# Kernel optimization log

Measured on AMD Instinct MI355X. Metric: run time of the kernel, lower is better.

Reference implementation:

```python
import jax, jax.numpy as jnp
import numpy as np

B, KLEN, QLEN = 16, 4096, 1
D_MODEL, HEADS, KERNELS = 1024, 8, 10
DIM = D_MODEL // HEADS  # 128
SCALE = 0.02


def setup_inputs() -> dict:
    key = jax.random.key(0)
    ks = jax.random.split(key, 12)
    return {
        "query": jax.random.normal(ks[0], (B, QLEN, D_MODEL), jnp.float32),
        "key_in": jax.random.normal(ks[1], (B, KLEN, D_MODEL), jnp.float32),
        "value": jax.random.normal(ks[2], (B, KLEN, D_MODEL), jnp.float32),
        "prev_align": jax.random.uniform(ks[3], (B, HEADS, KLEN), jnp.float32),
        # learned params
        "conv_w": jax.random.normal(ks[4], (KERNELS, HEADS, 3), jnp.float32) * SCALE,   # OIH, k=3
        "conv_b": jnp.zeros((KERNELS,), jnp.float32),
        "w_u": jax.random.normal(ks[5], (KERNELS, DIM), jnp.float32) * SCALE,
        "w_q": jax.random.normal(ks[6], (D_MODEL, HEADS * DIM), jnp.float32) * SCALE,
        "w_v": jax.random.normal(ks[7], (D_MODEL, HEADS * DIM), jnp.float32) * SCALE,
        "bias": jax.random.uniform(ks[8], (DIM,), jnp.float32, minval=-0.1, maxval=0.1),
        "score_w": jax.random.normal(ks[9], (DIM,), jnp.float32) * SCALE,
        "score_b": jnp.zeros((), jnp.float32),
    }


def reference(query, key_in, value, prev_align, conv_w, conv_b, w_u, w_q, w_v, bias, score_w, score_b):
    b, k_len = key_in.shape[0], key_in.shape[1]
    # location features: conv1d over k_len with heads as channels -> [B, KERNELS, k_len]
    loc = jax.lax.conv_general_dilated(
        prev_align, conv_w, window_strides=(1,), padding=[(1, 1)],
        dimension_numbers=("NCH", "OIH", "NCH")) + conv_b[None, :, None]
    loc_energy = jnp.tanh(jnp.einsum("bck,cd->bkd", loc, w_u))  # [B, k_len, DIM]
    # projections split into heads
    q = jnp.einsum("bqf,fe->bqe", query, w_q).reshape(b, QLEN, HEADS, DIM).transpose(0, 2, 1, 3)   # [B,H,1,DIM]
    k = jnp.einsum("bkf,fe->bke", key_in, w_v).reshape(b, k_len, HEADS, DIM).transpose(0, 2, 1, 3)  # [B,H,K,DIM]
    v = value.reshape(b, k_len, HEADS, DIM).transpose(0, 2, 1, 3)                                   # [B,H,K,DIM]
    # additive energy (q_len==1 broadcasts over keys)
    e = jnp.tanh(k + q + loc_energy[:, None] + bias)            # [B,H,K,DIM]
    score = jnp.einsum("bhkd,d->bhk", e, score_w) + score_b    # [B,H,K]
    align = jax.nn.softmax(score, axis=-1)
    context = jnp.einsum("bhk,bhkd->bhd", align, v).reshape(b * HEADS, DIM)
    return context, align
```

## Files before the change

kernel.cpp:

```cpp
#include <hip/hip_runtime.h>
#include <hip/hip_bf16.h>
#include <cstdint>

typedef __attribute__((ext_vector_type(8))) short bf16x8;
typedef __attribute__((ext_vector_type(4))) float f32x4;
typedef __attribute__((ext_vector_type(8))) unsigned short u16x8;
typedef __attribute__((ext_vector_type(4))) unsigned int u32x4;

__device__ __forceinline__ unsigned short f2bf(float f) {
    unsigned int u = __float_as_uint(f);
    unsigned int r = (u + 0x7fffu + ((u >> 16) & 1u)) >> 16;
    return (unsigned short)r;
}

__device__ __forceinline__ float tanh_fast(float x) {
    return 1.0f - 2.0f / (__expf(2.0f * x) + 1.0f);
}

#define GLDS(SRC, DST) __builtin_amdgcn_global_load_lds(                         \
        (const __attribute__((address_space(1))) void*)(SRC),                    \
        (__attribute__((address_space(3))) void*)(DST), 16, 0, 0)

__global__ __launch_bounds__(256) void wv_tile_kernel(
        const float* __restrict__ wv, unsigned short* __restrict__ out) {
    __shared__ float tile[32][129];
    const int h = blockIdx.x;
    const int kt = blockIdx.y;
    const int t = threadIdx.x;
    for (int i = t; i < 1024; i += 256) {
        const int fl = i >> 5;
        const int e4 = (i & 31) * 4;
        const float4 v = *reinterpret_cast<const float4*>(
            wv + (size_t)(kt * 32 + fl) * 1024 + h * 128 + e4);
        tile[fl][e4 + 0] = v.x; tile[fl][e4 + 1] = v.y;
        tile[fl][e4 + 2] = v.z; tile[fl][e4 + 3] = v.w;
    }
    __syncthreads();
#pragma unroll
    for (int cc2 = 0; cc2 < 2; ++cc2) {
        const int c = cc2 * 256 + t;
        const int cb = c >> 6, kg = (c >> 4) & 3, ccl = c & 15;
        const int e_local = cb * 16 + ccl;
        u16x8 u;
#pragma unroll
        for (int jj = 0; jj < 8; ++jj) u[jj] = f2bf(tile[kg * 8 + jj][e_local]);
        *reinterpret_cast<u16x8*>(out + (((size_t)h * 32 + kt) * 512 + c) * 8) = u;
    }
}

__global__ __launch_bounds__(128) void qproj_kernel(
        const float* __restrict__ query, const float* __restrict__ w_q,
        float* __restrict__ ws_q) {
    __shared__ float qs[1024];
    const int bh = blockIdx.x;
    const int b = bh >> 3, h = bh & 7;
    const int t = threadIdx.x;
    for (int i = t; i < 1024; i += 128) qs[i] = query[(size_t)b * 1024 + i];
    __syncthreads();
    float acc = 0.f;
    const float* wcol = w_q + h * 128 + t;
    for (int f = 0; f < 1024; ++f) acc = fmaf(qs[f], wcol[(size_t)f * 1024], acc);
    ws_q[(size_t)bh * 128 + t] = acc;
}

__global__ __launch_bounds__(256) void loc_le_kernel(
        const float* __restrict__ pa, const float* __restrict__ conv_w,
        const float* __restrict__ conv_b, const float* __restrict__ w_u,
        float* __restrict__ le) {
    __shared__ float pas[8][132];
    __shared__ float wu_s[10][128];
    __shared__ float cw[240];
    __shared__ float cb[16];
    const int b = blockIdx.x, k0 = blockIdx.y * 128;
    const int t = threadIdx.x;
    for (int i = t; i < 8 * 130; i += 256) {
        const int hh = i / 130, kk = i % 130;
        const int gk = k0 + kk - 1;
        pas[hh][kk] = (gk >= 0 && gk < 4096) ? pa[((size_t)(b * 8 + hh)) * 4096 + gk] : 0.f;
    }
    for (int i = t; i < 1280; i += 256) wu_s[i >> 7][i & 127] = w_u[i];
    if (t < 240) cw[t] = conv_w[t];
    if (t < 10) cb[t] = conv_b[t];
    __syncthreads();
    const int k = t >> 1;
    const int d0 = (t & 1) * 64;
    float lc[10];
#pragma unroll
    for (int c = 0; c < 10; ++c) {
        float acc = cb[c];
#pragma unroll
        for (int hh = 0; hh < 8; ++hh) {
            acc += pas[hh][k] * cw[(c * 8 + hh) * 3 + 0]
                 + pas[hh][k + 1] * cw[(c * 8 + hh) * 3 + 1]
                 + pas[hh][k + 2] * cw[(c * 8 + hh) * 3 + 2];
        }
        lc[c] = acc;
    }
    float* dst = le + ((size_t)(b * 4096) + k0 + k) * 128 + d0;
#pragma unroll
    for (int dd = 0; dd < 64; dd += 4) {
        float4 o;
#pragma unroll
        for (int jj = 0; jj < 4; ++jj) {
            float s = 0.f;
#pragma unroll
            for (int c = 0; c < 10; ++c) s += lc[c] * wu_s[c][d0 + dd + jj];
            ((float*)&o)[jj] = tanh_fast(s);
        }
        *reinterpret_cast<float4*>(dst + dd) = o;
    }
}

#define NT 32
__global__ __launch_bounds__(512) void gemm_score_kernel(
        const float* __restrict__ key_in, const unsigned short* __restrict__ wvT_tiled,
        const float* __restrict__ le,
        const float* __restrict__ ws_q, const float* __restrict__ bias,
        const float* __restrict__ score_w, const float* __restrict__ score_b,
        float* __restrict__ align_out) {
    __shared__ __align__(16) unsigned short As[3][4096];
    __shared__ __align__(16) unsigned short Bs[3][8192];
    __shared__ float qb_sm[256], sw_sm[128];
    __shared__ float partial[128][4];

    const int t = threadIdx.x;
    const int lane = t & 63, wid = t >> 6;
    const int wm = wid >> 2;
    const int wn = wid & 3;

    const int fid = blockIdx.x;
    const int x = fid & 7, j = fid >> 3;
    const int bm = x * 64 + (j >> 2);
    const int hp = j & 3;
    const int b = bm >> 5;
    const int kk0 = (bm & 31) << 7;

    if (t < 256) {
        const int hh = t >> 7, d = t & 127;
        qb_sm[t] = ws_q[(size_t)(b * 8 + hp * 2 + hh) * 128 + d] + bias[d];
        if (t < 128) sw_sm[t] = score_w[t];
    }

    const int r_ = t >> 2, ks = t & 3;
    const float* aRow = key_in + ((size_t)(b * 4096 + kk0) + r_) * 1024 + ks * 8;
    const int cW = (t >> 6) * 64 + ks * 16 + (r_ & 15);
    const int dst0 = (cW ^ (ks | ((ks & 1) << 2))) * 8;

    const int kgR = lane >> 4;
    const int laneSwz = lane ^ (kgR | ((kgR & 1) << 2));

    const unsigned short* bT = wvT_tiled
        + (size_t)(hp * 2 + (t >> 8)) * 131072 + (t & 255) * 8;
    const int dstB = (t >> 8) * 4096 + (t & 255) * 8;

    float4 st0, st1;

#define LOADA(KT) {                                                               \
        const float* p_ = aRow + (KT) * 32;                                       \
        st0 = *reinterpret_cast<const float4*>(p_);                               \
        st1 = *reinterpret_cast<const float4*>(p_ + 4); }

#define WRITEA(BUF) {                                                             \
        __hip_bfloat162 h0_ = __float22bfloat162_rn({st0.x, st0.y});              \
        __hip_bfloat162 h1_ = __float22bfloat162_rn({st0.z, st0.w});              \
        __hip_bfloat162 h2_ = __float22bfloat162_rn({st1.x, st1.y});              \
        __hip_bfloat162 h3_ = __float22bfloat162_rn({st1.z, st1.w});              \
        u32x4 u_;                                                                 \
        u_[0] = *reinterpret_cast<unsigned int*>(&h0_);                           \
        u_[1] = *reinterpret_cast<unsigned int*>(&h1_);                           \
        u_[2] = *reinterpret_cast<unsigned int*>(&h2_);                           \
        u_[3] = *reinterpret_cast<unsigned int*>(&h3_);                           \
        *reinterpret_cast<u32x4*>(&As[BUF][dst0]) = u_; }

#define STAGE_B(BUF, KT) {                                                        \
        GLDS(bT + (size_t)(KT) * 4096, &Bs[BUF][dstB]);                           \
        GLDS(bT + (size_t)(KT) * 4096 + 2048, &Bs[BUF][dstB + 2048]); }

    f32x4 acc[4][4] = {};

    LOADA(0);
    STAGE_B(0, 0);
    WRITEA(0);
    LOADA(1);

    for (int kt = 0; kt < NT; ++kt) {
        const int cur = kt % 3;
        const int nxt = (kt + 1) % 3;
        STAGE_B(nxt, (kt + 1) & (NT - 1));
        WRITEA(nxt);
        LOADA((kt + 2) & (NT - 1));
        asm volatile("s_waitcnt lgkmcnt(0)\n\t"
                     "s_barrier" ::: "memory");

        bf16x8 af[4], bg[4];
#pragma unroll
        for (int mf = 0; mf < 4; ++mf)
            af[mf] = *reinterpret_cast<const bf16x8*>(
                &As[cur][((wm * 4 + mf) * 64 + laneSwz) * 8]);
#pragma unroll
        for (int nf = 0; nf < 4; ++nf)
            bg[nf] = *reinterpret_cast<const bf16x8*>(
                &Bs[cur][(wn >> 1) * 4096 + ((wn & 1) * 4 + nf) * 512 + lane * 8]);
        __builtin_amdgcn_s_setprio(1);
#pragma unroll
        for (int mf = 0; mf < 4; ++mf)
#pragma unroll
            for (int nf = 0; nf < 4; ++nf)
                acc[mf][nf] = __builtin_amdgcn_mfma_f32_16x16x32_bf16(
                    af[mf], bg[nf], acc[mf][nf], 0, 0, 0);
        __builtin_amdgcn_s_setprio(0);
    }

    const float K2 = 2.8853900817779268f;
    const float sb = score_b[0];
    const int g = lane >> 4;
    const int l15 = lane & 15;
    float kqb[4], swv[4];
#pragma unroll
    for (int nf = 0; nf < 4; ++nf) {
        const int d128 = (wn & 1) * 64 + nf * 16 + l15;
        kqb[nf] = qb_sm[(wn >> 1) * 128 + d128] * K2;
        swv[nf] = sw_sm[d128];
    }
    const float* leB = le + ((size_t)(b * 4096 + kk0) + wm * 64 + g * 4) * 128
                       + (wn & 1) * 64 + l15;

#pragma unroll
    for (int mf = 0; mf < 4; ++mf) {
        float lv[16];
#pragma unroll
        for (int jj = 0; jj < 4; ++jj)
#pragma unroll
            for (int nf = 0; nf < 4; ++nf)
                lv[jj * 4 + nf] = leB[(size_t)(mf * 16 + jj) * 128 + nf * 16];
#pragma unroll
        for (int jj = 0; jj < 4; ++jj) {
            const int row_l = wm * 64 + mf * 16 + g * 4 + jj;
            float sum = 0.f;
#pragma unroll
            for (int nf = 0; nf < 4; ++nf) {
                const float m = fmaf(K2, lv[jj * 4 + nf], kqb[nf]);
                const float tt = fmaf(K2, acc[mf][nf][jj], m);
                const float y = __builtin_amdgcn_exp2f(tt);
                const float r = fmaf(-2.0f, __builtin_amdgcn_rcpf(y + 1.0f), 1.0f);
                sum = fmaf(r, swv[nf], sum);
            }
            sum += __shfl_xor(sum, 1);
            sum += __shfl_xor(sum, 2);
            sum += __shfl_xor(sum, 4);
            sum += __shfl_xor(sum, 8);
            if (l15 == 0) partial[row_l][wn] = sum;
        }
    }
    __syncthreads();
    if (t < 256) {
        const int r = t >> 1, hh = t & 1;
        const float sc = partial[r][hh * 2] + partial[r][hh * 2 + 1] + sb;
        align_out[(size_t)(b * 8 + hp * 2 + hh) * 4096 + kk0 + r] = sc;
    }
}

__global__ __launch_bounds__(256) void softmax_kernel(float* __restrict__ align_o) {
    const int bh = blockIdx.x;
    float* row = align_o + (size_t)bh * 4096;
    const int t = threadIdx.x;
    float v[16];
    float m = -1e30f;
#pragma unroll
    for (int i = 0; i < 16; ++i) {
        v[i] = row[i * 256 + t];
        m = fmaxf(m, v[i]);
    }
#pragma unroll
    for (int off = 32; off; off >>= 1) m = fmaxf(m, __shfl_xor(m, off));
    __shared__ float sm[4], ss[4];
    const int wid = t >> 6;
    if ((t & 63) == 0) sm[wid] = m;
    __syncthreads();
    m = fmaxf(fmaxf(sm[0], sm[1]), fmaxf(sm[2], sm[3]));
    float s = 0.f;
#pragma unroll
    for (int i = 0; i < 16; ++i) {
        v[i] = __expf(v[i] - m);
        s += v[i];
    }
#pragma unroll
    for (int off = 32; off; off >>= 1) s += __shfl_xor(s, off);
    if ((t & 63) == 0) ss[wid] = s;
    __syncthreads();
    s = ss[0] + ss[1] + ss[2] + ss[3];
    const float inv = 1.f / s;
#pragma unroll
    for (int i = 0; i < 16; ++i) row[i * 256 + t] = v[i] * inv;
}

__global__ __launch_bounds__(256) void ctx_partial_kernel(
        const float* __restrict__ value, const float* __restrict__ align_o,
        float* __restrict__ pctx) {
    const int s = blockIdx.x;
    const int bh = blockIdx.y;
    const int b = bh >> 3, h = bh & 7;
    const int t = threadIdx.x;
    const int d4 = (t & 31) * 4;
    const int kg = t >> 5;
    const float* arow = align_o + (size_t)bh * 4096 + s * 128;
    const float* vbase = value + ((size_t)(b * 4096 + s * 128)) * 1024 + h * 128 + d4;
    float4 acc = {0.f, 0.f, 0.f, 0.f};
    for (int i = 0; i < 16; ++i) {
        const int kk = i * 8 + kg;
        const float a = arow[kk];
        const float4 v = *reinterpret_cast<const float4*>(vbase + (size_t)kk * 1024);
        acc.x += a * v.x; acc.y += a * v.y; acc.z += a * v.z; acc.w += a * v.w;
    }
    __shared__ float sm2[8][128];
    *reinterpret_cast<float4*>(&sm2[kg][d4]) = acc;
    __syncthreads();
    if (t < 128) {
        float s0 = 0.f;
#pragma unroll
        for (int gg = 0; gg < 8; ++gg) s0 += sm2[gg][t];
        pctx[((size_t)bh * 32 + s) * 128 + t] = s0;
    }
}

__global__ __launch_bounds__(128) void ctx_reduce_kernel(
        const float* __restrict__ pctx, float* __restrict__ out) {
    const int bh = blockIdx.x;
    const int t = threadIdx.x;
    float acc = 0.f;
    for (int s2 = 0; s2 < 32; ++s2) acc += pctx[((size_t)bh * 32 + s2) * 128 + t];
    out[(size_t)bh * 128 + t] = acc;
}

extern "C" void kernel_launch(void* const* d_in, const int* in_sizes, int n_in,
                              void* d_out, int out_size, void* d_ws, size_t ws_size,
                              hipStream_t stream) {
    const float* query   = (const float*)d_in[0];
    const float* key_in  = (const float*)d_in[1];
    const float* value   = (const float*)d_in[2];
    const float* pa      = (const float*)d_in[3];
    const float* conv_w  = (const float*)d_in[4];
    const float* conv_b  = (const float*)d_in[5];
    const float* w_u     = (const float*)d_in[6];
    const float* w_q     = (const float*)d_in[7];
    const float* w_v     = (const float*)d_in[8];
    const float* bias    = (const float*)d_in[9];
    const float* score_w = (const float*)d_in[10];
    const float* score_b = (const float*)d_in[11];

    float* out = (float*)d_out;
    float* ctx_out = out;
    float* align_out = out + 16384;

    char* ws = (char*)d_ws;
    const size_t OFF_Q    = 0;
    const size_t OFF_WVT  = 65536;
    const size_t OFF_PCTX = OFF_WVT + 2097152;
    const size_t OFF_LE   = OFF_PCTX + 2097152;

    float* ws_q            = (float*)(ws + OFF_Q);
    unsigned short* ws_wvT = (unsigned short*)(ws + OFF_WVT);
    float* ws_pctx         = (float*)(ws + OFF_PCTX);
    float* ws_le           = (float*)(ws + OFF_LE);

    hipLaunchKernelGGL(wv_tile_kernel, dim3(8, 32), dim3(256), 0, stream, w_v, ws_wvT);
    hipLaunchKernelGGL(qproj_kernel, dim3(128), dim3(128), 0, stream, query, w_q, ws_q);
    hipLaunchKernelGGL(loc_le_kernel, dim3(16, 32), dim3(256), 0, stream,
                       pa, conv_w, conv_b, w_u, ws_le);
    hipLaunchKernelGGL(gemm_score_kernel, dim3(2048), dim3(512), 0, stream,
                       key_in, ws_wvT, ws_le, ws_q, bias, score_w, score_b, align_out);
    hipLaunchKernelGGL(softmax_kernel, dim3(128), dim3(256), 0, stream, align_out);
    hipLaunchKernelGGL(ctx_partial_kernel, dim3(32, 128), dim3(256), 0, stream, value, align_out, ws_pctx);
    hipLaunchKernelGGL(ctx_reduce_kernel, dim3(128), dim3(128), 0, stream, ws_pctx, ctx_out);
}
```

Measured before the change: 302.8 us.

## Merge prep kernels into one launch and deepen B-tile prefetch to two stages

Folds the W_v tiling, query projection, and location-energy kernels into one launch that branches on block index, removing two launch gaps and letting the three independent jobs run together. In the GEMM main loop, the B-tile async global-to-LDS copy is now issued two iterations ahead, after the barrier, using the third buffer. This gives the copy more time in flight before it is needed. It depends on the existing lgkmcnt wait and barrier being enough to order the async LDS writes against reads of the buffer being refilled.

```diff
diff --git a/kernel.cpp b/kernel.cpp
--- a/kernel.cpp
+++ b/kernel.cpp
@@ -21,93 +21,95 @@
         (const __attribute__((address_space(1))) void*)(SRC),                    \
         (__attribute__((address_space(3))) void*)(DST), 16, 0, 0)
 
-__global__ __launch_bounds__(256) void wv_tile_kernel(
-        const float* __restrict__ wv, unsigned short* __restrict__ out) {
-    __shared__ float tile[32][129];
-    const int h = blockIdx.x;
-    const int kt = blockIdx.y;
-    const int t = threadIdx.x;
-    for (int i = t; i < 1024; i += 256) {
-        const int fl = i >> 5;
-        const int e4 = (i & 31) * 4;
-        const float4 v = *reinterpret_cast<const float4*>(
-            wv + (size_t)(kt * 32 + fl) * 1024 + h * 128 + e4);
-        tile[fl][e4 + 0] = v.x; tile[fl][e4 + 1] = v.y;
-        tile[fl][e4 + 2] = v.z; tile[fl][e4 + 3] = v.w;
-    }
-    __syncthreads();
-#pragma unroll
-    for (int cc2 = 0; cc2 < 2; ++cc2) {
-        const int c = cc2 * 256 + t;
-        const int cb = c >> 6, kg = (c >> 4) & 3, ccl = c & 15;
-        const int e_local = cb * 16 + ccl;
-        u16x8 u;
-#pragma unroll
-        for (int jj = 0; jj < 8; ++jj) u[jj] = f2bf(tile[kg * 8 + jj][e_local]);
-        *reinterpret_cast<u16x8*>(out + (((size_t)h * 32 + kt) * 512 + c) * 8) = u;
-    }
-}
-
-__global__ __launch_bounds__(128) void qproj_kernel(
+__global__ __launch_bounds__(256) void prep_kernel(
+        const float* __restrict__ wv, unsigned short* __restrict__ wvT,
         const float* __restrict__ query, const float* __restrict__ w_q,
-        float* __restrict__ ws_q) {
-    __shared__ float qs[1024];
-    const int bh = blockIdx.x;
-    const int b = bh >> 3, h = bh & 7;
-    const int t = threadIdx.x;
-    for (int i = t; i < 1024; i += 128) qs[i] = query[(size_t)b * 1024 + i];
-    __syncthreads();
-    float acc = 0.f;
-    const float* wcol = w_q + h * 128 + t;
-    for (int f = 0; f < 1024; ++f) acc = fmaf(qs[f], wcol[(size_t)f * 1024], acc);
-    ws_q[(size_t)bh * 128 + t] = acc;
-}
-
-__global__ __launch_bounds__(256) void loc_le_kernel(
+        float* __restrict__ ws_q,
         const float* __restrict__ pa, const float* __restrict__ conv_w,
         const float* __restrict__ conv_b, const float* __restrict__ w_u,
         float* __restrict__ le) {
-    __shared__ float pas[8][132];
-    __shared__ float wu_s[10][128];
-    __shared__ float cw[240];
-    __shared__ float cb[16];
-    const int b = blockIdx.x, k0 = blockIdx.y * 128;
-    const int t = threadIdx.x;
-    for (int i = t; i < 8 * 130; i += 256) {
-        const int hh = i / 130, kk = i % 130;
-        const int gk = k0 + kk - 1;
-        pas[hh][kk] = (gk >= 0 && gk < 4096) ? pa[((size_t)(b * 8 + hh)) * 4096 + gk] : 0.f;
-    }
-    for (int i = t; i < 1280; i += 256) wu_s[i >> 7][i & 127] = w_u[i];
-    if (t < 240) cw[t] = conv_w[t];
-    if (t < 10) cb[t] = conv_b[t];
-    __syncthreads();
-    const int k = t >> 1;
-    const int d0 = (t & 1) * 64;
-    float lc[10];
-#pragma unroll
-    for (int c = 0; c < 10; ++c) {
-        float acc = cb[c];
-#pragma unroll
-        for (int hh = 0; hh < 8; ++hh) {
-            acc += pas[hh][k] * cw[(c * 8 + hh) * 3 + 0]
-                 + pas[hh][k + 1] * cw[(c * 8 + hh) * 3 + 1]
-                 + pas[hh][k + 2] * cw[(c * 8 + hh) * 3 + 2];
-        }
-        lc[c] = acc;
-    }
-    float* dst = le + ((size_t)(b * 4096) + k0 + k) * 128 + d0;
-#pragma unroll
-    for (int dd = 0; dd < 64; dd += 4) {
-        float4 o;
-#pragma unroll
-        for (int jj = 0; jj < 4; ++jj) {
-            float s = 0.f;
-#pragma unroll
-            for (int c = 0; c < 10; ++c) s += lc[c] * wu_s[c][d0 + dd + jj];
-            ((float*)&o)[jj] = tanh_fast(s);
-        }
-        *reinterpret_cast<float4*>(dst + dd) = o;
+    __shared__ __align__(16) char smem[16640];
+    const int bid = blockIdx.x;
+    const int t = threadIdx.x;
+
+    if (bid < 256) {
+        float (*tile)[129] = reinterpret_cast<float(*)[129]>(smem);
+        const int h = bid >> 5, kt = bid & 31;
+        for (int i = t; i < 1024; i += 256) {
+            const int fl = i >> 5;
+            const int e4 = (i & 31) * 4;
+            const float4 v = *reinterpret_cast<const float4*>(
+                wv + (size_t)(kt * 32 + fl) * 1024 + h * 128 + e4);
+            tile[fl][e4 + 0] = v.x; tile[fl][e4 + 1] = v.y;
+            tile[fl][e4 + 2] = v.z; tile[fl][e4 + 3] = v.w;
+        }
+        __syncthreads();
+#pragma unroll
+        for (int cc2 = 0; cc2 < 2; ++cc2) {
+            const int c = cc2 * 256 + t;
+            const int cb = c >> 6, kg = (c >> 4) & 3, ccl = c & 15;
+            const int e_local = cb * 16 + ccl;
+            u16x8 u;
+#pragma unroll
+            for (int jj = 0; jj < 8; ++jj) u[jj] = f2bf(tile[kg * 8 + jj][e_local]);
+            *reinterpret_cast<u16x8*>(wvT + (((size_t)h * 32 + kt) * 512 + c) * 8) = u;
+        }
+    } else if (bid < 384) {
+        float* qs = reinterpret_cast<float*>(smem);
+        const int bh = bid - 256;
+        const int b = bh >> 3, h = bh & 7;
+        for (int i = t; i < 1024; i += 256) qs[i] = query[(size_t)b * 1024 + i];
+        __syncthreads();
+        if (t < 128) {
+            float acc = 0.f;
+            const float* wcol = w_q + h * 128 + t;
+            for (int f = 0; f < 1024; ++f) acc = fmaf(qs[f], wcol[(size_t)f * 1024], acc);
+            ws_q[(size_t)bh * 128 + t] = acc;
+        }
+    } else {
+        float* pas = reinterpret_cast<float*>(smem);
+        float* wu_s = pas + 1056;
+        float* cw = wu_s + 1280;
+        float* cb = cw + 240;
+        const int idx = bid - 384;
+        const int b = idx >> 5, k0 = (idx & 31) * 128;
+        for (int i = t; i < 8 * 130; i += 256) {
+            const int hh = i / 130, kk = i % 130;
+            const int gk = k0 + kk - 1;
+            pas[hh * 132 + kk] = (gk >= 0 && gk < 4096)
+                ? pa[((size_t)(b * 8 + hh)) * 4096 + gk] : 0.f;
+        }
+        for (int i = t; i < 1280; i += 256) wu_s[i] = w_u[i];
+        if (t < 240) cw[t] = conv_w[t];
+        if (t < 10) cb[t] = conv_b[t];
+        __syncthreads();
+        const int k = t >> 1;
+        const int d0 = (t & 1) * 64;
+        float lc[10];
+#pragma unroll
+        for (int c = 0; c < 10; ++c) {
+            float acc = cb[c];
+#pragma unroll
+            for (int hh = 0; hh < 8; ++hh) {
+                acc += pas[hh * 132 + k] * cw[(c * 8 + hh) * 3 + 0]
+                     + pas[hh * 132 + k + 1] * cw[(c * 8 + hh) * 3 + 1]
+                     + pas[hh * 132 + k + 2] * cw[(c * 8 + hh) * 3 + 2];
+            }
+            lc[c] = acc;
+        }
+        float* dst = le + ((size_t)(b * 4096) + k0 + k) * 128 + d0;
+#pragma unroll
+        for (int dd = 0; dd < 64; dd += 4) {
+            float4 o;
+#pragma unroll
+            for (int jj = 0; jj < 4; ++jj) {
+                float s = 0.f;
+#pragma unroll
+                for (int c = 0; c < 10; ++c) s += lc[c] * wu_s[c * 128 + d0 + dd + jj];
+                ((float*)&o)[jj] = tanh_fast(s);
+            }
+            *reinterpret_cast<float4*>(dst + dd) = o;
+        }
     }
 }
 
@@ -180,17 +182,19 @@
 
     LOADA(0);
     STAGE_B(0, 0);
+    STAGE_B(1, 1);
     WRITEA(0);
     LOADA(1);
 
     for (int kt = 0; kt < NT; ++kt) {
         const int cur = kt % 3;
         const int nxt = (kt + 1) % 3;
-        STAGE_B(nxt, (kt + 1) & (NT - 1));
+        const int pre = (kt + 2) % 3;
         WRITEA(nxt);
         LOADA((kt + 2) & (NT - 1));
         asm volatile("s_waitcnt lgkmcnt(0)\n\t"
                      "s_barrier" ::: "memory");
+        STAGE_B(pre, (kt + 2) & (NT - 1));
 
         bf16x8 af[4], bg[4];
 #pragma unroll
@@ -363,9 +367,8 @@
     float* ws_pctx         = (float*)(ws + OFF_PCTX);
     float* ws_le           = (float*)(ws + OFF_LE);
 
-    hipLaunchKernelGGL(wv_tile_kernel, dim3(8, 32), dim3(256), 0, stream, w_v, ws_wvT);
-    hipLaunchKernelGGL(qproj_kernel, dim3(128), dim3(128), 0, stream, query, w_q, ws_q);
-    hipLaunchKernelGGL(loc_le_kernel, dim3(16, 32), dim3(256), 0, stream,
+    hipLaunchKernelGGL(prep_kernel, dim3(896), dim3(256), 0, stream,
+                       w_v, ws_wvT, query, w_q, ws_q,
                        pa, conv_w, conv_b, w_u, ws_le);
     hipLaunchKernelGGL(gemm_score_kernel, dim3(2048), dim3(512), 0, stream,
                        key_in, ws_wvT, ws_le, ws_q, bias, score_w, score_b, align_out);
```

Result: no change. 297.8 us (-1.7%).
